# Optimization experiments

Hardware: AMD Instinct MI355X
Metric: run time of the kernel (lower is better)

## Reference

```python
import jax, jax.numpy as jnp
import numpy as np

D_MODEL, N, L_MAX, BATCH = 512, 64, 2048, 8


def _hippo_pq_lambda(n):
    # HiPPO-LegS matrix -> NPLR decomposition (numpy, done once at setup)
    i = np.arange(n)
    A = np.sqrt(2 * i + 1)[:, None] * np.sqrt(2 * i + 1)[None, :]
    A = np.tril(A, -1) + np.diag(i + 1.0)
    p0 = 0.5 * np.sqrt(2 * np.arange(1, n + 1) - 1.0)
    q0 = 2.0 * p0
    S = -A + p0[:, None] * q0[None, :]
    lam, V = np.linalg.eig(S)
    Vc = V.conj().T
    p = Vc @ p0.astype(np.complex128)
    q = Vc @ q0.astype(np.complex128)
    return lam, p, q


def _c2r(x):
    return np.stack([x.real, x.imag], axis=-1).astype(np.float32)


def setup_inputs() -> dict:
    key = jax.random.key(0)
    ks = jax.random.split(key, 6)
    lam, p, q = _hippo_pq_lambda(N)
    log_step_scale = float(np.log(0.1) - np.log(0.001))
    xavier_std = (2.0 / (D_MODEL + N)) ** 0.5
    return {
        "u": jax.random.normal(ks[0], (BATCH, L_MAX, D_MODEL), jnp.float32),
        "lam": jnp.asarray(_c2r(lam)),            # (N, 2) complex-as-real
        "p": jnp.asarray(_c2r(p)),                # (N, 2)
        "q": jnp.asarray(_c2r(q)),                # (N, 2)
        "B": jax.random.normal(ks[1], (D_MODEL, N, 2), jnp.float32) * xavier_std,
        "Ct": jax.random.normal(ks[2], (D_MODEL, N, 2), jnp.float32) * xavier_std,
        "D": jnp.ones((D_MODEL,), jnp.float32),
        "log_step": jax.random.uniform(ks[3], (D_MODEL,), jnp.float32) * log_step_scale + float(np.log(0.001)),
        "W": jax.random.normal(ks[4], (D_MODEL, D_MODEL), jnp.float32) / (D_MODEL ** 0.5),
        "b": jnp.zeros((D_MODEL,), jnp.float32),
        "gamma": jnp.ones((D_MODEL,), jnp.float32),
        "beta": jnp.zeros((D_MODEL,), jnp.float32),
    }


def _cplx(x):
    return x[..., 0] + 1j * x[..., 1]


def _s4_kernel(lam, p, q, B, Ct, step, l_max):
    # Generating function of the DPLR SSM kernel evaluated at roots of unity,
    # then inverse FFT -> length-l_max convolution kernel K, shape (d_model, l_max).
    omega = jnp.exp(2j * jnp.pi * jnp.arange(l_max) / l_max)  # (L,)
    a0, a1 = jnp.conj(Ct), jnp.conj(q)   # (d,n), (n,)
    b0, b1 = B, p                        # (d,n), (n,)
    v = jnp.stack([
        a0 * b0,
        a0 * b1[None, :],
        a1[None, :] * b0,
        jnp.broadcast_to((a1 * b1)[None, :], B.shape),
    ])  # (4, d, n)
    f = (2.0 / step)[:, None] * ((1.0 - omega) / (1.0 + omega))[None, :]  # (d, L)
    r = 1.0 / (f[:, :, None] - lam)      # (d, L, n)  -- dominant intermediate
    k = jnp.einsum('kdn,dln->kdl', v, r) # 4 Cauchy dots in one contraction
    at_roots = (2.0 / (1.0 + omega)) * (k[0] - k[1] * (1.0 / (1.0 + k[3])) * k[2])
    return jnp.fft.ifft(at_roots, n=l_max, axis=-1).real  # (d, L)


def _s4_block(u, lam, p, q, B, Ct, D, log_step, W, b, gamma, beta):
    L = u.shape[1]
    K = _s4_kernel(_cplx(lam), _cplx(p), _cplx(q), _cplx(B), _cplx(Ct), jnp.exp(log_step), L)
    # non-circular convolution via zero-padded FFT
    ud = jnp.fft.rfft(jnp.pad(u, ((0, 0), (0, L), (0, 0))), axis=1)   # (b, L+1, d)
    Kd = jnp.fft.rfft(jnp.pad(K, ((0, 0), (0, L))), axis=-1)          # (d, L+1)
    y = jnp.fft.irfft(ud * Kd.T[None], axis=1)[:, :L, :] + D * u      # S4Layer out
    y = jax.nn.gelu(y, approximate=False)                             # nn.GELU (exact)
    y = y @ W.T + b                                                   # nn.Linear
    y = y + u                                                         # Residual
    mu = jnp.mean(y, axis=-1, keepdims=True)                          # LayerNorm (post)
    var = jnp.mean((y - mu) ** 2, axis=-1, keepdims=True)
    return (y - mu) * jax.lax.rsqrt(var + 1e-5) * gamma + beta


def reference(u, lam, p, q, B, Ct, D, log_step, W, b, gamma, beta):
    return _s4_block(u, lam, p, q, B, Ct, D, log_step, W, b, gamma, beta)
```

## Files before the change

kernel.cpp:

```cpp
#include <hip/hip_runtime.h>
#include <math.h>

#define DM 512
#define NS 64
#define LS 2048
#define NB 8
#define LF 4096
#define LSP (LS + (LS>>5))

typedef float2 cf;
using bf16x8 = __attribute__((ext_vector_type(8))) short;
using f32x4  = __attribute__((ext_vector_type(4))) float;

__device__ __forceinline__ cf cmul(cf a, cf b){ return make_float2(a.x*b.x - a.y*b.y, a.x*b.y + a.y*b.x); }
__device__ __forceinline__ cf cadd(cf a, cf b){ return make_float2(a.x+b.x, a.y+b.y); }
__device__ __forceinline__ cf csub(cf a, cf b){ return make_float2(a.x-b.x, a.y-b.y); }
__device__ __forceinline__ cf cconjf(cf a){ return make_float2(a.x, -a.y); }
__device__ __forceinline__ cf cscalef(cf a, float s){ return make_float2(a.x*s, a.y*s); }
__device__ __forceinline__ cf cdiv_fast(cf a, cf b){
  float inv = __builtin_amdgcn_rcpf(b.x*b.x + b.y*b.y);
  return make_float2((a.x*b.x + a.y*b.y)*inv, (a.y*b.x - a.x*b.y)*inv);
}

__device__ __forceinline__ float gelu_f(float x){
  return 0.5f*x*(1.0f + erff(x*0.7071067811865475f));
}

__device__ __forceinline__ ushort f2bf(float x){
  uint u = __float_as_uint(x);
  return (ushort)((u + 0x7fffu + ((u>>16)&1u)) >> 16);
}

__device__ __forceinline__ int lp(int x){ return x + (x >> 5); }

__device__ __forceinline__ float2 f2add(float2 a, float2 b){ return make_float2(a.x+b.x, a.y+b.y); }
__device__ __forceinline__ float2 f2mul(float2 a, float2 b){ return make_float2(a.x*b.x, a.y*b.y); }
__device__ __forceinline__ float2 f2fma(float2 a, float2 b, float2 c){
  return make_float2(fmaf(a.x,b.x,c.x), fmaf(a.y,b.y,c.y));
}
__device__ __forceinline__ float2 splat2(float s){ return make_float2(s,s); }
__device__ __forceinline__ float2 rcp2(float2 a){
  return make_float2(__builtin_amdgcn_rcpf(a.x), __builtin_amdgcn_rcpf(a.y));
}

template<int N, int T, bool INV>
__device__ float2* fft_stockham4(float2* a, float2* b, int tid) {
  float2* src = a; float2* dst = b;
  const float base = (INV ? 6.283185307179586f : -6.283185307179586f) / (float)N;
  const float sg = INV ? 1.0f : -1.0f;
  int m = 1;
  while (m * 4 <= N) {
    __syncthreads();
    #pragma unroll
    for (int ii = 0; ii < N/4/T; ii++) {
      int i = tid + ii*T;
      int j = i & ~(m-1);
      float2 c0 = src[i];
      float2 c1 = src[i + N/4];
      float2 c2 = src[i + 2*(N/4)];
      float2 c3 = src[i + 3*(N/4)];
      float2 s02 = cadd(c0,c2), d02 = csub(c0,c2);
      float2 s13 = cadd(c1,c3), d13 = csub(c1,c3);
      float2 jd13 = make_float2(-sg*d13.y, sg*d13.x);
      float2 y0 = cadd(s02, s13);
      float2 y1 = cadd(d02, jd13);
      float2 y2 = csub(s02, s13);
      float2 y3 = csub(d02, jd13);
      float ang = base * (float)j;
      float sn, cs; __sincosf(ang, &sn, &cs);
      float2 w1 = make_float2(cs, sn);
      float2 w2 = cmul(w1, w1);
      float2 w3 = cmul(w2, w1);
      int o = i + 3*j;
      dst[o]       = y0;
      dst[o + m]   = cmul(y1, w1);
      dst[o + 2*m] = cmul(y2, w2);
      dst[o + 3*m] = cmul(y3, w3);
    }
    float2* tswap = src; src = dst; dst = tswap;
    m <<= 2;
  }
  if (m * 2 <= N) {
    __syncthreads();
    #pragma unroll
    for (int ii = 0; ii < N/2/T; ii++) {
      int i = tid + ii*T;
      int j = i & ~(m-1);
      float2 c0 = src[i], c1 = src[i + N/2];
      float ang = base * (float)j;
      float sn, cs; __sincosf(ang, &sn, &cs);
      float2 sum = cadd(c0,c1), dif = csub(c0,c1);
      dst[i + j]     = sum;
      dst[i + j + m] = cmul(dif, make_float2(cs,sn));
    }
    float2* tswap = src; src = dst; dst = tswap;
    m <<= 1;
  }
  __syncthreads();
  return src;
}

template<int N, int T, bool INV>
__device__ float2* fft_stockham8(float2* a, float2* b, int tid) {
  float2* src = a; float2* dst = b;
  const float base = (INV ? 6.283185307179586f : -6.283185307179586f) / (float)N;
  const float sg = INV ? 1.0f : -1.0f;
  const float C8 = 0.70710678118654752f;
  int m = 1;
  while (m * 8 <= N) {
    __syncthreads();
    #pragma unroll
    for (int ii = 0; ii < N/8/T; ii++) {
      int i = tid + ii*T;
      int j = i & ~(m-1);
      float2 c[8];
      #pragma unroll
      for (int t = 0; t < 8; t++) c[t] = src[lp(i + t*(N/8))];
      float2 s0=cadd(c[0],c[4]), d0=csub(c[0],c[4]);
      float2 s1=cadd(c[1],c[5]), d1=csub(c[1],c[5]);
      float2 s2=cadd(c[2],c[6]), d2=csub(c[2],c[6]);
      float2 s3=cadd(c[3],c[7]), d3=csub(c[3],c[7]);
      float2 t1 = make_float2(C8*(d1.x - sg*d1.y), C8*(d1.y + sg*d1.x));
      float2 t2 = make_float2(-sg*d2.y, sg*d2.x);
      float2 t3 = make_float2(-C8*(d3.x + sg*d3.y), C8*(sg*d3.x - d3.y));
      float2 es=cadd(s0,s2), ed=csub(s0,s2), fs=cadd(s1,s3), fd=csub(s1,s3);
      float2 je = make_float2(-sg*fd.y, sg*fd.x);
      float2 y0=cadd(es,fs), y4=csub(es,fs);
      float2 y2=cadd(ed,je), y6=csub(ed,je);
      float2 os=cadd(d0,t2), od=csub(d0,t2), ps=cadd(t1,t3), pd=csub(t1,t3);
      float2 jo = make_float2(-sg*pd.y, sg*pd.x);
      float2 y1=cadd(os,ps), y5=csub(os,ps);
      float2 y3=cadd(od,jo), y7=csub(od,jo);
      float ang = base*(float)j;
      float sn, cs; __sincosf(ang, &sn, &cs);
      float2 w1 = make_float2(cs, sn);
      float2 w2 = cmul(w1,w1), w3 = cmul(w2,w1), w4 = cmul(w2,w2);
      float2 w5 = cmul(w4,w1), w6 = cmul(w4,w2), w7 = cmul(w4,w3);
      int o = i + 7*j;
      dst[lp(o)]       = y0;
      dst[lp(o + m)]   = cmul(y1,w1);
      dst[lp(o + 2*m)] = cmul(y2,w2);
      dst[lp(o + 3*m)] = cmul(y3,w3);
      dst[lp(o + 4*m)] = cmul(y4,w4);
      dst[lp(o + 5*m)] = cmul(y5,w5);
      dst[lp(o + 6*m)] = cmul(y6,w6);
      dst[lp(o + 7*m)] = cmul(y7,w7);
    }
    float2* tswap = src; src = dst; dst = tswap;
    m <<= 3;
  }
  if (m * 4 <= N) {
    __syncthreads();
    #pragma unroll
    for (int ii = 0; ii < N/4/T; ii++) {
      int i = tid + ii*T;
      int j = i & ~(m-1);
      float2 c0 = src[lp(i)];
      float2 c1 = src[lp(i + N/4)];
      float2 c2 = src[lp(i + 2*(N/4))];
      float2 c3 = src[lp(i + 3*(N/4))];
      float2 s02 = cadd(c0,c2), d02 = csub(c0,c2);
      float2 s13 = cadd(c1,c3), d13 = csub(c1,c3);
      float2 jd13 = make_float2(-sg*d13.y, sg*d13.x);
      float2 y0 = cadd(s02, s13);
      float2 y1 = cadd(d02, jd13);
      float2 y2 = csub(s02, s13);
      float2 y3 = csub(d02, jd13);
      float ang = base * (float)j;
      float sn, cs; __sincosf(ang, &sn, &cs);
      float2 w1 = make_float2(cs, sn);
      float2 w2 = cmul(w1, w1);
      float2 w3 = cmul(w2, w1);
      int o = i + 3*j;
      dst[lp(o)]       = y0;
      dst[lp(o + m)]   = cmul(y1, w1);
      dst[lp(o + 2*m)] = cmul(y2, w2);
      dst[lp(o + 3*m)] = cmul(y3, w3);
    }
    float2* tswap = src; src = dst; dst = tswap;
    m <<= 2;
  }
  if (m * 2 <= N) {
    __syncthreads();
    #pragma unroll
    for (int ii = 0; ii < N/2/T; ii++) {
      int i = tid + ii*T;
      int j = i & ~(m-1);
      float2 c0 = src[lp(i)], c1 = src[lp(i + N/2)];
      float ang = base * (float)j;
      float sn, cs; __sincosf(ang, &sn, &cs);
      float2 sum = cadd(c0,c1), dif = csub(c0,c1);
      dst[lp(i + j)]     = sum;
      dst[lp(i + j + m)] = cmul(dif, make_float2(cs,sn));
    }
    float2* tswap = src; src = dst; dst = tswap;
    m <<= 1;
  }
  __syncthreads();
  return src;
}

__global__ __launch_bounds__(256) void transpose_kernel(
    const float* __restrict__ u, float* __restrict__ ut)
{
  __shared__ float tile[32][33];
  int b  = blockIdx.z;
  int t0 = blockIdx.x * 32;
  int d0 = blockIdx.y * 32;
  int tx = threadIdx.x & 31;
  int ty = threadIdx.x >> 5;
  #pragma unroll
  for (int r = 0; r < 32; r += 8)
    tile[ty + r][tx] = u[((size_t)b*LS + t0 + ty + r)*DM + d0 + tx];
  __syncthreads();
  #pragma unroll
  for (int r = 0; r < 32; r += 8)
    ut[((size_t)b*DM + d0 + ty + r)*LS + t0 + tx] = tile[tx][ty + r];
}

__global__ __launch_bounds__(256) void cauchy_kernel(
    const float* __restrict__ lam_g, const float* __restrict__ p_g,
    const float* __restrict__ q_g,   const float* __restrict__ B_g,
    const float* __restrict__ Ct_g,  const float* __restrict__ logstep_g,
    float2* __restrict__ at)
{
  __shared__ float tab[NS][12];
  int d     = blockIdx.x;
  int chunk = blockIdx.y;
  int tid = threadIdx.x;
  float tos = 2.0f / expf(logstep_g[d]);
  float invtos = __builtin_amdgcn_rcpf(tos);

  if (tid < NS) {
    int n = tid;
    float lx = lam_g[2*n], ly = lam_g[2*n+1];
    cf pn   = make_float2(p_g[2*n],   p_g[2*n+1]);
    cf qn   = make_float2(q_g[2*n],   q_g[2*n+1]);
    cf Bdn  = make_float2(B_g[(d*NS+n)*2],  B_g[(d*NS+n)*2+1]);
    cf Cdn  = make_float2(Ct_g[(d*NS+n)*2], Ct_g[(d*NS+n)*2+1]);
    cf a0 = cconjf(Cdn);
    cf a1 = cconjf(qn);
    cf w0 = cmul(a0, Bdn);
    cf w1 = cmul(a0, pn);
    cf w2 = cmul(a1, Bdn);
    cf w3 = cmul(a1, pn);
    tab[n][0] = -lx;  tab[n][1] = ly;   tab[n][2] = lx*lx; tab[n][3] = w0.x;
    tab[n][4] = w0.y; tab[n][5] = w1.x; tab[n][6] = w1.y;  tab[n][7] = w2.x;
    tab[n][8] = w2.y; tab[n][9] = w3.x; tab[n][10] = w3.y; tab[n][11] = 0.f;
  }

  float2 g2[2];
  #pragma unroll
  for (int sp = 0; sp < 2; sp++) {
    float gg[2];
    #pragma unroll
    for (int h = 0; h < 2; h++) {
      int l = chunk*1024 + (2*sp + h)*256 + tid;
      float half_ang = 3.14159265358979323846f * (float)l / (float)LS;
      float sn, cs;
      sincosf(half_ang, &sn, &cs);
      gg[h] = tos * (sn / cs);
    }
    g2[sp] = make_float2(gg[0], gg[1]);
  }
  __syncthreads();

  float2 k0x[2], k0y[2], k1x[2], k1y[2], k2x[2], k2y[2], k3x[2], k3y[2];
  #pragma unroll
  for (int sp = 0; sp < 2; sp++) {
    k0x[sp] = splat2(0.f); k0y[sp] = splat2(0.f);
    k1x[sp] = splat2(0.f); k1y[sp] = splat2(0.f);
    k2x[sp] = splat2(0.f); k2y[sp] = splat2(0.f);
    k3x[sp] = splat2(0.f); k3y[sp] = splat2(0.f);
  }

  #pragma unroll 2
  for (int n = 0; n < NS; n++) {
    float4 t0 = *reinterpret_cast<const float4*>(&tab[n][0]);
    float4 t1 = *reinterpret_cast<const float4*>(&tab[n][4]);
    float4 t2 = *reinterpret_cast<const float4*>(&tab[n][8]);
    #pragma unroll
    for (int sp = 0; sp < 2; sp++) {
      float2 e   = f2add(g2[sp], splat2(t0.y));
      float2 mag = f2fma(e, e, splat2(t0.z));
      float2 inv = rcp2(mag);
      float2 rx  = f2mul(splat2(t0.x), inv);
      float2 ry  = f2mul(e, inv);
      k0x[sp] = f2fma(splat2(t0.w), rx, k0x[sp]);
      k0x[sp] = f2fma(splat2(-t1.x), ry, k0x[sp]);
      k0y[sp] = f2fma(splat2(t0.w), ry, k0y[sp]);
      k0y[sp] = f2fma(splat2(t1.x), rx, k0y[sp]);
      k1x[sp] = f2fma(splat2(t1.y), rx, k1x[sp]);
      k1x[sp] = f2fma(splat2(-t1.z), ry, k1x[sp]);
      k1y[sp] = f2fma(splat2(t1.y), ry, k1y[sp]);
      k1y[sp] = f2fma(splat2(t1.z), rx, k1y[sp]);
      k2x[sp] = f2fma(splat2(t1.w), rx, k2x[sp]);
      k2x[sp] = f2fma(splat2(-t2.x), ry, k2x[sp]);
      k2y[sp] = f2fma(splat2(t1.w), ry, k2y[sp]);
      k2y[sp] = f2fma(splat2(t2.x), rx, k2y[sp]);
      k3x[sp] = f2fma(splat2(t2.y), rx, k3x[sp]);
      k3x[sp] = f2fma(splat2(-t2.z), ry, k3x[sp]);
      k3y[sp] = f2fma(splat2(t2.y), ry, k3y[sp]);
      k3y[sp] = f2fma(splat2(t2.z), rx, k3y[sp]);
    }
  }

  #pragma unroll
  for (int sp = 0; sp < 2; sp++) {
    #pragma unroll
    for (int h = 0; h < 2; h++) {
      int l = chunk*1024 + (2*sp + h)*256 + tid;
      float gv = (h == 0) ? g2[sp].x : g2[sp].y;
      cf k0 = make_float2(h==0?k0x[sp].x:k0x[sp].y, h==0?k0y[sp].x:k0y[sp].y);
      cf k1 = make_float2(h==0?k1x[sp].x:k1x[sp].y, h==0?k1y[sp].x:k1y[sp].y);
      cf k2 = make_float2(h==0?k2x[sp].x:k2x[sp].y, h==0?k2y[sp].x:k2y[sp].y);
      cf k3 = make_float2(h==0?k3x[sp].x:k3x[sp].y, h==0?k3y[sp].x:k3y[sp].y);
      cf t1c = cdiv_fast(cmul(k1, k2), make_float2(1.0f + k3.x, k3.y));
      cf inner = csub(k0, t1c);
      cf c2 = make_float2(1.0f, -gv * invtos);
      at[(size_t)d*LS + l] = cmul(c2, inner);
    }
  }
}

__global__ __launch_bounds__(256) void kfft_kernel(
    const float2* __restrict__ at, float2* __restrict__ Kf)
{
  __shared__ float2 bufA[LSP];
  __shared__ float2 bufB[LSP];
  int tid = threadIdx.x;
  int d0 = blockIdx.x * 2;
  const float2* at0 = at + (size_t)d0*LS;
  const float2* at1 = at0 + LS;
  float2* Kf0 = Kf + (size_t)d0*LF;
  float2* Kf1 = Kf0 + LF;

  #pragma unroll
  for (int s = 0; s < 8; s++) {
    int k = tid + s*256;
    int nk = (LS - k) & (LS - 1);
    cf a0k = at0[k], a0n = at0[nk];
    cf a1k = at1[k], a1n = at1[nk];
    cf H0 = make_float2(0.5f*(a0k.x + a0n.x), 0.5f*(a0k.y - a0n.y));
    cf H1 = make_float2(0.5f*(a1k.x + a1n.x), 0.5f*(a1k.y - a1n.y));
    Kf0[k] = H0;
    Kf1[k] = H1;
    bufA[lp(k)] = make_float2(H0.x - H1.y, H0.y + H1.x);
  }
  float2* res = fft_stockham8<LS, 256, true>(bufA, bufB, tid);
  float2* other = (res == bufA) ? bufB : bufA;
  #pragma unroll
  for (int s = 0; s < 8; s++) {
    int t = tid + s*256;
    float ang = 3.14159265358979323846f * (float)t / (float)LS;
    float sn, cs;
    __sincosf(ang, &sn, &cs);
    cf Kc = cscalef(res[lp(t)], 1.0f/(float)LS);
    other[lp(t)] = cmul(Kc, make_float2(cs, -sn));
  }
  float2* G = fft_stockham8<LS, 256, false>(other, res, tid);
  #pragma unroll
  for (int s = 0; s < 4; s++) {
    int k = tid + s*256;
    int rk = LS - 1 - k;
    cf Gk = G[lp(k)], Gr = G[lp(rk)];
    cf F0 = make_float2(0.5f*(Gk.x + Gr.x), 0.5f*(Gk.y - Gr.y));
    cf F1 = make_float2(0.5f*(Gk.y + Gr.y), 0.5f*(Gr.x - Gk.x));
    Kf0[LS + k]  = F0;
    Kf0[LS + rk] = cconjf(F0);
    Kf1[LS + k]  = F1;
    Kf1[LS + rk] = cconjf(F1);
  }
}

__global__ __launch_bounds__(512) void conv_kernel(
    const float* __restrict__ ut, const float2* __restrict__ Kf,
    const float* __restrict__ Dv, ushort* __restrict__ gb)
{
  __shared__ float2 bufA[LS];
  __shared__ float2 bufB[LS];
  int tid = threadIdx.x;
  int d0 = blockIdx.x * 2;
  int b  = blockIdx.y;
  const float* u0p = ut + ((size_t)b*DM + d0)*LS;
  const float* u1p = u0p + LS;
  const float2* Kf0 = Kf + (size_t)d0 * LF;
  const float2* Kf1 = Kf0 + LF;
  float u0r[4], u1r[4];
  #pragma unroll
  for (int s = 0; s < 4; s++) {
    int t = tid + s*512;
    u0r[s] = u0p[t]; u1r[s] = u1p[t];
    bufA[t] = make_float2(u0r[s], u1r[s]);
  }

  float2* Z  = fft_stockham4<LS, 512, false>(bufA, bufB, tid);
  float2* Wb = (Z == bufA) ? bufB : bufA;
  #pragma unroll
  for (int s = 0; s < 4; s++) {
    int mq = tid + s*512;
    int mm = (LS - mq) & (LS - 1);
    cf Za = Z[mq], Zb = Z[mm];
    cf U0 = make_float2(0.5f*(Za.x + Zb.x), 0.5f*(Za.y - Zb.y));
    cf U1 = make_float2(0.5f*(Za.y + Zb.y), 0.5f*(Zb.x - Za.x));
    cf Y0 = cmul(U0, Kf0[mq]);
    cf Y1 = cmul(U1, Kf1[mq]);
    Wb[mq] = make_float2(Y0.x - Y1.y, Y0.y + Y1.x);
  }
  float2* A = fft_stockham4<LS, 512, true>(Wb, Z, tid);
  float2 areg[4];
  #pragma unroll
  for (int s = 0; s < 4; s++) areg[s] = A[tid + s*512];

  float2* st = (A == bufA) ? bufB : bufA;
  #pragma unroll
  for (int s = 0; s < 4; s++) {
    int t = tid + s*512;
    float ang = -3.14159265358979323846f * (float)t / (float)LS;
    float sn, cs; __sincosf(ang, &sn, &cs);
    cf z = make_float2(u0r[s], u1r[s]);
    st[t] = cmul(z, make_float2(cs, sn));
  }
  float2* Z2  = fft_stockham4<LS, 512, false>(st, A, tid);
  float2* Wb2 = (Z2 == bufA) ? bufB : bufA;
  #pragma unroll
  for (int s = 0; s < 4; s++) {
    int mq = tid + s*512;
    int mm = LS - 1 - mq;
    cf Za = Z2[mq], Zb = Z2[mm];
    cf U0 = make_float2(0.5f*(Za.x + Zb.x), 0.5f*(Za.y - Zb.y));
    cf U1 = make_float2(0.5f*(Za.y + Zb.y), 0.5f*(Zb.x - Za.x));
    cf Y0 = cmul(U0, Kf0[LS + mq]);
    cf Y1 = cmul(U1, Kf1[LS + mq]);
    Wb2[mq] = make_float2(Y0.x - Y1.y, Y0.y + Y1.x);
  }
  float2* C = fft_stockham4<LS, 512, true>(Wb2, Z2, tid);

  float dv0 = Dv[d0], dv1 = Dv[d0+1];
  ushort* g0 = gb + ((size_t)b*DM + d0)*LS;
  ushort* g1 = g0 + LS;
  #pragma unroll
  for (int s = 0; s < 4; s++) {
    int t = tid + s*512;
    float ang = 3.14159265358979323846f * (float)t / (float)LS;
    float sn, cs; __sincosf(ang, &sn, &cs);
    cf c = C[t];
    cf bb = cmul(c, make_float2(cs, sn));
    float y0 = (areg[s].x + bb.x) * (1.0f/LF) + dv0 * u0r[s];
    float y1 = (areg[s].y + bb.y) * (1.0f/LF) + dv1 * u1r[s];
    g0[t] = f2bf(gelu_f(y0));
    g1[t] = f2bf(gelu_f(y1));
  }
}

__global__ __launch_bounds__(256) void transposeT_kernel(
    const ushort* __restrict__ gb, ushort* __restrict__ gt)
{
  __shared__ ushort tile[64][65];
  int b  = blockIdx.z;
  int t0 = blockIdx.x * 64;
  int d0 = blockIdx.y * 64;
  int tx = threadIdx.x & 31;
  int ty = threadIdx.x >> 5;
  #pragma unroll
  for (int r = 0; r < 8; r++) {
    int d = ty + r*8;
    uint v = *reinterpret_cast<const uint*>(&gb[((size_t)b*DM + d0 + d)*LS + t0 + tx*2]);
    tile[d][tx*2]   = (ushort)(v & 0xffffu);
    tile[d][tx*2+1] = (ushort)(v >> 16);
  }
  __syncthreads();
  #pragma unroll
  for (int r = 0; r < 8; r++) {
    int t = ty + r*8;
    uint lo = tile[tx*2][t];
    uint hi = tile[tx*2+1][t];
    *reinterpret_cast<uint*>(&gt[((size_t)b*LS + t0 + t)*DM + d0 + tx*2]) = lo | (hi << 16);
  }
}

__global__ __launch_bounds__(256) void wb_kernel(
    const float* __restrict__ W, ushort* __restrict__ Wb)
{
  int i = (blockIdx.x*256 + threadIdx.x)*4;
  float4 v = *reinterpret_cast<const float4*>(W + i);
  uint2 o;
  o.x = (uint)f2bf(v.x) | ((uint)f2bf(v.y) << 16);
  o.y = (uint)f2bf(v.z) | ((uint)f2bf(v.w) << 16);
  *reinterpret_cast<uint2*>(Wb + i) = o;
}

__global__ __launch_bounds__(256) void mfma_gemm_kernel(
    const ushort* __restrict__ gt, const ushort* __restrict__ Wbm,
    const float* __restrict__ bias, const float* __restrict__ u,
    float* __restrict__ out)
{
  __shared__ ushort As[128*64];
  __shared__ ushort Bs[128*64];
  int tid = threadIdx.x;
  int b  = blockIdx.z;
  int t0 = blockIdx.x * 128;
  int j0 = blockIdx.y * 128;
  int wid = tid >> 6, lane = tid & 63;
  int wm = wid >> 1, wn = wid & 1;
  int m = lane & 15, q = lane >> 4;

  f32x4 acc[4][4];
  #pragma unroll
  for (int i = 0; i < 4; i++)
    #pragma unroll
    for (int j = 0; j < 4; j++)
      acc[i][j] = (f32x4){0.f, 0.f, 0.f, 0.f};

  const ushort* Ag = gt + ((size_t)b*LS + t0)*DM;

  for (int k0 = 0; k0 < DM; k0 += 64) {
    #pragma unroll
    for (int i = 0; i < 4; i++) {
      int idx = tid + i*256;
      int r = idx >> 3, g = idx & 7;
      uint4 va = *reinterpret_cast<const uint4*>(Ag + (size_t)r*DM + k0 + g*8);
      *reinterpret_cast<uint4*>(&As[r*64 + ((g ^ (r&7))*8)]) = va;
      uint4 vb = *reinterpret_cast<const uint4*>(Wbm + (size_t)(j0 + r)*DM + k0 + g*8);
      *reinterpret_cast<uint4*>(&Bs[r*64 + ((g ^ (r&7))*8)]) = vb;
    }
    __syncthreads();
    #pragma unroll
    for (int kk = 0; kk < 64; kk += 32) {
      int gk = (kk >> 3) + q;
      bf16x8 af[4], bfr[4];
      #pragma unroll
      for (int mi = 0; mi < 4; mi++) {
        int row = wm*64 + mi*16 + m;
        af[mi] = *reinterpret_cast<const bf16x8*>(&As[row*64 + ((gk ^ (row&7))*8)]);
      }
      #pragma unroll
      for (int ni = 0; ni < 4; ni++) {
        int row = wn*64 + ni*16 + m;
        bfr[ni] = *reinterpret_cast<const bf16x8*>(&Bs[row*64 + ((gk ^ (row&7))*8)]);
      }
      #pragma unroll
      for (int mi = 0; mi < 4; mi++)
        #pragma unroll
        for (int ni = 0; ni < 4; ni++)
          acc[mi][ni] = __builtin_amdgcn_mfma_f32_16x16x32_bf16(af[mi], bfr[ni], acc[mi][ni], 0, 0, 0);
    }
    __syncthreads();
  }

  #pragma unroll
  for (int mi = 0; mi < 4; mi++) {
    #pragma unroll
    for (int ni = 0; ni < 4; ni++) {
      int col = j0 + wn*64 + ni*16 + m;
      float bb = bias[col];
      #pragma unroll
      for (int jj = 0; jj < 4; jj++) {
        int row = t0 + wm*64 + mi*16 + q*4 + jj;
        size_t off = ((size_t)b*LS + row)*DM + col;
        out[off] = acc[mi][ni][jj] + bb + u[off];
      }
    }
  }
}

__global__ __launch_bounds__(256) void ln_kernel(
    float* __restrict__ out, const float* __restrict__ gamma,
    const float* __restrict__ beta)
{
  int lane = threadIdx.x & 63;
  size_t row = (size_t)blockIdx.x * 4 + (threadIdx.x >> 6);
  float* p = out + row * DM;
  float4 v0 = *reinterpret_cast<float4*>(p + lane*8);
  float4 v1 = *reinterpret_cast<float4*>(p + lane*8 + 4);
  float sum = v0.x+v0.y+v0.z+v0.w + v1.x+v1.y+v1.z+v1.w;
  float sq  = v0.x*v0.x+v0.y*v0.y+v0.z*v0.z+v0.w*v0.w
            + v1.x*v1.x+v1.y*v1.y+v1.z*v1.z+v1.w*v1.w;
  #pragma unroll
  for (int off = 32; off >= 1; off >>= 1) {
    sum += __shfl_xor(sum, off, 64);
    sq  += __shfl_xor(sq,  off, 64);
  }
  float mu  = sum * (1.0f/DM);
  float var = sq  * (1.0f/DM) - mu*mu;
  float rs  = rsqrtf(var + 1e-5f);
  float4 g0 = *reinterpret_cast<const float4*>(gamma + lane*8);
  float4 g1 = *reinterpret_cast<const float4*>(gamma + lane*8 + 4);
  float4 b0 = *reinterpret_cast<const float4*>(beta + lane*8);
  float4 b1 = *reinterpret_cast<const float4*>(beta + lane*8 + 4);
  v0.x = (v0.x - mu)*rs*g0.x + b0.x;
  v0.y = (v0.y - mu)*rs*g0.y + b0.y;
  v0.z = (v0.z - mu)*rs*g0.z + b0.z;
  v0.w = (v0.w - mu)*rs*g0.w + b0.w;
  v1.x = (v1.x - mu)*rs*g1.x + b1.x;
  v1.y = (v1.y - mu)*rs*g1.y + b1.y;
  v1.z = (v1.z - mu)*rs*g1.z + b1.z;
  v1.w = (v1.w - mu)*rs*g1.w + b1.w;
  *reinterpret_cast<float4*>(p + lane*8)     = v0;
  *reinterpret_cast<float4*>(p + lane*8 + 4) = v1;
}

extern "C" void kernel_launch(void* const* d_in, const int* in_sizes, int n_in,
                              void* d_out, int out_size, void* d_ws, size_t ws_size,
                              hipStream_t stream) {
  const float* u       = (const float*)d_in[0];
  const float* lam     = (const float*)d_in[1];
  const float* p       = (const float*)d_in[2];
  const float* q       = (const float*)d_in[3];
  const float* B       = (const float*)d_in[4];
  const float* Ct      = (const float*)d_in[5];
  const float* Dv      = (const float*)d_in[6];
  const float* logstep = (const float*)d_in[7];
  const float* W       = (const float*)d_in[8];
  const float* bias    = (const float*)d_in[9];
  const float* gamma   = (const float*)d_in[10];
  const float* beta    = (const float*)d_in[11];
  float* out = (float*)d_out;

  char* wsb = (char*)d_ws;
  float2* Kf  = (float2*)wsb;
  ushort* gb  = (ushort*)(wsb + (size_t)16*1024*1024);
  ushort* Wbm = (ushort*)(wsb + (size_t)16*1024*1024);
  float2* at  = (float2*)(wsb + (size_t)32*1024*1024);
  ushort* gt  = (ushort*)(wsb + (size_t)32*1024*1024);
  float* ut = (float*)d_out;

  transpose_kernel<<<dim3(LS/32, DM/32, NB), 256, 0, stream>>>(u, ut);
  cauchy_kernel<<<dim3(DM, 2), 256, 0, stream>>>(lam, p, q, B, Ct, logstep, at);
  kfft_kernel<<<dim3(DM/2), 256, 0, stream>>>(at, Kf);
  conv_kernel<<<dim3(DM/2, NB), 512, 0, stream>>>(ut, Kf, Dv, gb);
  transposeT_kernel<<<dim3(LS/64, DM/64, NB), 256, 0, stream>>>(gb, gt);
  wb_kernel<<<dim3(DM*DM/1024), 256, 0, stream>>>(W, Wbm);
  mfma_gemm_kernel<<<dim3(LS/128, DM/128, NB), 256, 0, stream>>>(gt, Wbm, bias, u, out);
  ln_kernel<<<dim3(NB*LS/4), 256, 0, stream>>>(out, gamma, beta);
}
```

Baseline: 160.2 us.

## Fuse LayerNorm into GEMM epilogue with full-row output tiles

The GEMM is retiled so each 512-thread block computes 64 full output rows across all 512 columns. This lets LayerNorm statistics be reduced in the epilogue through shuffles and a small shared buffer, and the separate LN kernel is removed. That saves one full read and write of the fp32 output plus a launch. In exchange, each block stages the whole W slice (64 KB of B tile per k-step), and the grid shrinks to 256 blocks, which lowers occupancy and parallelism.

```diff
diff --git a/kernel.cpp b/kernel.cpp
--- a/kernel.cpp
+++ b/kernel.cpp
@@ -490,114 +490,130 @@
   *reinterpret_cast<uint2*>(Wb + i) = o;
 }
 
-__global__ __launch_bounds__(256) void mfma_gemm_kernel(
+__global__ __launch_bounds__(512) void gemm_ln_kernel(
     const ushort* __restrict__ gt, const ushort* __restrict__ Wbm,
     const float* __restrict__ bias, const float* __restrict__ u,
+    const float* __restrict__ gamma, const float* __restrict__ beta,
     float* __restrict__ out)
 {
-  __shared__ ushort As[128*64];
-  __shared__ ushort Bs[128*64];
+  __shared__ ushort As[64*64];
+  __shared__ ushort Bs[512*64];
+  __shared__ float red[2][64][4];
   int tid = threadIdx.x;
-  int b  = blockIdx.z;
-  int t0 = blockIdx.x * 128;
-  int j0 = blockIdx.y * 128;
+  int b  = blockIdx.y;
+  int t0 = blockIdx.x * 64;
   int wid = tid >> 6, lane = tid & 63;
-  int wm = wid >> 1, wn = wid & 1;
+  int wm = wid >> 2, wn = wid & 3;
   int m = lane & 15, q = lane >> 4;
 
-  f32x4 acc[4][4];
-  #pragma unroll
-  for (int i = 0; i < 4; i++)
-    #pragma unroll
-    for (int j = 0; j < 4; j++)
+  f32x4 acc[2][8];
+  #pragma unroll
+  for (int i = 0; i < 2; i++)
+    #pragma unroll
+    for (int j = 0; j < 8; j++)
       acc[i][j] = (f32x4){0.f, 0.f, 0.f, 0.f};
 
   const ushort* Ag = gt + ((size_t)b*LS + t0)*DM;
 
   for (int k0 = 0; k0 < DM; k0 += 64) {
-    #pragma unroll
-    for (int i = 0; i < 4; i++) {
-      int idx = tid + i*256;
-      int r = idx >> 3, g = idx & 7;
+    {
+      int r = tid >> 3, g = tid & 7;
       uint4 va = *reinterpret_cast<const uint4*>(Ag + (size_t)r*DM + k0 + g*8);
       *reinterpret_cast<uint4*>(&As[r*64 + ((g ^ (r&7))*8)]) = va;
-      uint4 vb = *reinterpret_cast<const uint4*>(Wbm + (size_t)(j0 + r)*DM + k0 + g*8);
+    }
+    #pragma unroll
+    for (int i = 0; i < 8; i++) {
+      int idx = tid + i*512;
+      int r = idx >> 3, g = idx & 7;
+      uint4 vb = *reinterpret_cast<const uint4*>(Wbm + (size_t)r*DM + k0 + g*8);
       *reinterpret_cast<uint4*>(&Bs[r*64 + ((g ^ (r&7))*8)]) = vb;
     }
     __syncthreads();
     #pragma unroll
     for (int kk = 0; kk < 64; kk += 32) {
       int gk = (kk >> 3) + q;
-      bf16x8 af[4], bfr[4];
-      #pragma unroll
-      for (int mi = 0; mi < 4; mi++) {
-        int row = wm*64 + mi*16 + m;
+      bf16x8 af[2], bfr[8];
+      #pragma unroll
+      for (int mi = 0; mi < 2; mi++) {
+        int row = wm*32 + mi*16 + m;
         af[mi] = *reinterpret_cast<const bf16x8*>(&As[row*64 + ((gk ^ (row&7))*8)]);
       }
       #pragma unroll
-      for (int ni = 0; ni < 4; ni++) {
-        int row = wn*64 + ni*16 + m;
+      for (int ni = 0; ni < 8; ni++) {
+        int row = wn*128 + ni*16 + m;
         bfr[ni] = *reinterpret_cast<const bf16x8*>(&Bs[row*64 + ((gk ^ (row&7))*8)]);
       }
       #pragma unroll
-      for (int mi = 0; mi < 4; mi++)
+      for (int mi = 0; mi < 2; mi++)
         #pragma unroll
-        for (int ni = 0; ni < 4; ni++)
+        for (int ni = 0; ni < 8; ni++)
           acc[mi][ni] = __builtin_amdgcn_mfma_f32_16x16x32_bf16(af[mi], bfr[ni], acc[mi][ni], 0, 0, 0);
     }
     __syncthreads();
   }
 
-  #pragma unroll
-  for (int mi = 0; mi < 4; mi++) {
-    #pragma unroll
-    for (int ni = 0; ni < 4; ni++) {
-      int col = j0 + wn*64 + ni*16 + m;
+  float sum_[2][4], sq_[2][4];
+  #pragma unroll
+  for (int mi = 0; mi < 2; mi++)
+    #pragma unroll
+    for (int jj = 0; jj < 4; jj++) { sum_[mi][jj] = 0.f; sq_[mi][jj] = 0.f; }
+
+  #pragma unroll
+  for (int mi = 0; mi < 2; mi++) {
+    #pragma unroll
+    for (int ni = 0; ni < 8; ni++) {
+      int col = wn*128 + ni*16 + m;
       float bb = bias[col];
       #pragma unroll
       for (int jj = 0; jj < 4; jj++) {
-        int row = t0 + wm*64 + mi*16 + q*4 + jj;
+        int row = t0 + wm*32 + mi*16 + q*4 + jj;
+        float y = acc[mi][ni][jj] + bb + u[((size_t)b*LS + row)*DM + col];
+        acc[mi][ni][jj] = y;
+        sum_[mi][jj] += y;
+        sq_[mi][jj]  += y*y;
+      }
+    }
+  }
+  #pragma unroll
+  for (int mi = 0; mi < 2; mi++)
+    #pragma unroll
+    for (int jj = 0; jj < 4; jj++) {
+      #pragma unroll
+      for (int off = 1; off < 16; off <<= 1) {
+        sum_[mi][jj] += __shfl_xor(sum_[mi][jj], off, 64);
+        sq_[mi][jj]  += __shfl_xor(sq_[mi][jj],  off, 64);
+      }
+    }
+  if (m == 0) {
+    #pragma unroll
+    for (int mi = 0; mi < 2; mi++)
+      #pragma unroll
+      for (int jj = 0; jj < 4; jj++) {
+        int rowl = wm*32 + mi*16 + q*4 + jj;
+        red[0][rowl][wn] = sum_[mi][jj];
+        red[1][rowl][wn] = sq_[mi][jj];
+      }
+  }
+  __syncthreads();
+  #pragma unroll
+  for (int mi = 0; mi < 2; mi++) {
+    #pragma unroll
+    for (int jj = 0; jj < 4; jj++) {
+      int rowl = wm*32 + mi*16 + q*4 + jj;
+      float s  = red[0][rowl][0] + red[0][rowl][1] + red[0][rowl][2] + red[0][rowl][3];
+      float s2 = red[1][rowl][0] + red[1][rowl][1] + red[1][rowl][2] + red[1][rowl][3];
+      float mu  = s * (1.0f/DM);
+      float var = s2 * (1.0f/DM) - mu*mu;
+      float rs  = rsqrtf(var + 1e-5f);
+      int row = t0 + rowl;
+      #pragma unroll
+      for (int ni = 0; ni < 8; ni++) {
+        int col = wn*128 + ni*16 + m;
         size_t off = ((size_t)b*LS + row)*DM + col;
-        out[off] = acc[mi][ni][jj] + bb + u[off];
+        out[off] = (acc[mi][ni][jj] - mu) * rs * gamma[col] + beta[col];
       }
     }
   }
-}
-
-__global__ __launch_bounds__(256) void ln_kernel(
-    float* __restrict__ out, const float* __restrict__ gamma,
-    const float* __restrict__ beta)
-{
-  int lane = threadIdx.x & 63;
-  size_t row = (size_t)blockIdx.x * 4 + (threadIdx.x >> 6);
-  float* p = out + row * DM;
-  float4 v0 = *reinterpret_cast<float4*>(p + lane*8);
-  float4 v1 = *reinterpret_cast<float4*>(p + lane*8 + 4);
-  float sum = v0.x+v0.y+v0.z+v0.w + v1.x+v1.y+v1.z+v1.w;
-  float sq  = v0.x*v0.x+v0.y*v0.y+v0.z*v0.z+v0.w*v0.w
-            + v1.x*v1.x+v1.y*v1.y+v1.z*v1.z+v1.w*v1.w;
-  #pragma unroll
-  for (int off = 32; off >= 1; off >>= 1) {
-    sum += __shfl_xor(sum, off, 64);
-    sq  += __shfl_xor(sq,  off, 64);
-  }
-  float mu  = sum * (1.0f/DM);
-  float var = sq  * (1.0f/DM) - mu*mu;
-  float rs  = rsqrtf(var + 1e-5f);
-  float4 g0 = *reinterpret_cast<const float4*>(gamma + lane*8);
-  float4 g1 = *reinterpret_cast<const float4*>(gamma + lane*8 + 4);
-  float4 b0 = *reinterpret_cast<const float4*>(beta + lane*8);
-  float4 b1 = *reinterpret_cast<const float4*>(beta + lane*8 + 4);
-  v0.x = (v0.x - mu)*rs*g0.x + b0.x;
-  v0.y = (v0.y - mu)*rs*g0.y + b0.y;
-  v0.z = (v0.z - mu)*rs*g0.z + b0.z;
-  v0.w = (v0.w - mu)*rs*g0.w + b0.w;
-  v1.x = (v1.x - mu)*rs*g1.x + b1.x;
-  v1.y = (v1.y - mu)*rs*g1.y + b1.y;
-  v1.z = (v1.z - mu)*rs*g1.z + b1.z;
-  v1.w = (v1.w - mu)*rs*g1.w + b1.w;
-  *reinterpret_cast<float4*>(p + lane*8)     = v0;
-  *reinterpret_cast<float4*>(p + lane*8 + 4) = v1;
 }
 
 extern "C" void kernel_launch(void* const* d_in, const int* in_sizes, int n_in,
@@ -631,6 +647,5 @@
   conv_kernel<<<dim3(DM/2, NB), 512, 0, stream>>>(ut, Kf, Dv, gb);
   transposeT_kernel<<<dim3(LS/64, DM/64, NB), 256, 0, stream>>>(gb, gt);
   wb_kernel<<<dim3(DM*DM/1024), 256, 0, stream>>>(W, Wbm);
-  mfma_gemm_kernel<<<dim3(LS/128, DM/128, NB), 256, 0, stream>>>(gt, Wbm, bias, u, out);
-  ln_kernel<<<dim3(NB*LS/4), 256, 0, stream>>>(out, gamma, beta);
-}
+  gemm_ln_kernel<<<dim3(LS/64, NB), 512, 0, stream>>>(gt, Wbm, bias, u, gamma, beta, out);
+}
```

Result: faster. 153.8 us (-4.0%).
